# Performance work log

Hardware: AMD Instinct MI355X
Metric: run time of the kernel (lower is better)

## Reference

```python
import jax, jax.numpy as jnp
import numpy as np

N, FIN, H, C, D = 50000, 128, 4, 64, 4
E = 800000


def leaky_relu(x, slope):
    return jnp.where(x >= 0, x, slope * x)


def gat_layer(x, src, dst, W, A, att_src, att_dst, bias):
    # x: [N, Fin]; W: [Fin, H*C]; A: [Fin, H*D]; att_*: [H, D]; bias: [C]
    n = x.shape[0]
    h = (x @ W).reshape(n, H, -1)          # [N, H, C] message features
    a = (x @ A).reshape(n, H, -1)          # [N, H, D] attention features
    alpha_src = jnp.einsum('nhd,hd->nh', a, att_src)   # [N, H]
    alpha_dst = jnp.einsum('nhd,hd->nh', a, att_dst)   # [N, H]
    e = leaky_relu(alpha_src[src] + alpha_dst[dst], 0.2)  # [E, H]
    # edge softmax over incoming edges of each destination node
    m = jax.ops.segment_max(e, dst, num_segments=n)       # [N, H]
    ex = jnp.exp(e - m[dst])                               # [E, H]
    denom = jax.ops.segment_sum(ex, dst, num_segments=n)  # [N, H]
    w = ex / denom[dst]                                    # [E, H]
    msg = h[src] * w[..., None]                            # [E, H, C]
    out = jax.ops.segment_sum(msg, dst, num_segments=n)   # [N, H, C]
    return out.mean(axis=1) + bias                         # head-average -> [N, C]


def setup_inputs() -> dict:
    key = jax.random.key(0)
    ks = jax.random.split(key, 12)
    x = jax.random.normal(ks[0], (N, FIN), dtype=jnp.float32)
    edge_index = jax.random.randint(ks[1], (2, E), 0, N, dtype=jnp.int64)
    s = 0.05
    return {
        'x': x,
        'edge_index': edge_index,
        'W1': jax.random.normal(ks[2], (FIN, H * C), dtype=jnp.float32) * s,
        'A1': jax.random.normal(ks[3], (FIN, H * D), dtype=jnp.float32) * s,
        'att_src1': jax.random.normal(ks[4], (H, D), dtype=jnp.float32) * s,
        'att_dst1': jax.random.normal(ks[5], (H, D), dtype=jnp.float32) * s,
        'b1': jnp.zeros((C,), dtype=jnp.float32),
        'W2': jax.random.normal(ks[6], (C, H * C), dtype=jnp.float32) * s,
        'A2': jax.random.normal(ks[7], (C, H * D), dtype=jnp.float32) * s,
        'att_src2': jax.random.normal(ks[8], (H, D), dtype=jnp.float32) * s,
        'att_dst2': jax.random.normal(ks[9], (H, D), dtype=jnp.float32) * s,
        'b2': jnp.zeros((C,), dtype=jnp.float32),
    }


def reference(x, edge_index, W1, A1, att_src1, att_dst1, b1, W2, A2, att_src2, att_dst2, b2):
    src, dst = edge_index[0], edge_index[1]
    x = gat_layer(x, src, dst, W1, A1, att_src1, att_dst1, b1)
    x = leaky_relu(x, 0.1)
    x = gat_layer(x, src, dst, W2, A2, att_src2, att_dst2, b2)
    x = leaky_relu(x, 0.1)
    return x
```

## Files before the change

kernel.cpp:

```cpp
#include <hip/hip_runtime.h>


#define N_NODES 50000
#define N_EDGES 800000
#define CAP 64
#define NB_SC4 782
#define NB_NODE1 782

typedef __attribute__((ext_vector_type(8))) short short8;
typedef __attribute__((ext_vector_type(8))) _Float16 f16x8;
typedef __attribute__((ext_vector_type(4))) float f32x4;
typedef __attribute__((ext_vector_type(8))) unsigned short ushort8;
typedef __attribute__((ext_vector_type(4))) unsigned short us4v;

__device__ __forceinline__ float bf2f(unsigned short u){
  return __uint_as_float(((unsigned int)u) << 16);
}
__device__ __forceinline__ unsigned short f2bf(float f){
  unsigned int u = __float_as_uint(f);
  u = (u + 0x7FFFu + ((u >> 16) & 1u)) >> 16;
  return (unsigned short)u;
}
__device__ __forceinline__ float ldf(const void* p, int i, bool bf){
  return bf ? bf2f(((const unsigned short*)p)[i]) : ((const float*)p)[i];
}

struct SetupPtrs {
  const void *W1, *A1, *aS1, *aD1, *b1, *W2, *A2, *aS2, *aD2, *b2, *x;
};

__global__ __launch_bounds__(256) void k_setup(SetupPtrs S,
    _Float16* __restrict__ Wb1f, _Float16* __restrict__ Wb2f,
    unsigned short* __restrict__ Bsd1f, unsigned short* __restrict__ Bsd2f,
    float* __restrict__ bc1, float* __restrict__ bc2,
    int* __restrict__ flag)
{
  __shared__ int sbf;
  const int tid = threadIdx.x;
  if (tid < 64){
    unsigned int w = ((const unsigned int*)S.x)[tid] & 0xFFFFu;
    unsigned int e = (w >> 7) & 0xFFu;
    bool hit = (e >= 100u && e <= 135u);
    unsigned long long m = __ballot(hit);
    if (tid == 0) sbf = (__popcll(m) > 40) ? 1 : 0;
  }
  __syncthreads();
  const bool bf = (sbf != 0);
  const int bw = blockIdx.x;
  if (bw < 128){
    int t = bw * 256 + tid;
    int j = t & 7, lane = (t >> 3) & 63, kt = (t >> 9) & 15, nt = t >> 13;
    int q = kt * 32 + (lane >> 4) * 8 + j;
    int c = nt * 16 + (lane & 15);
    int h = q >> 7, f = q & 127;
    Wb1f[t] = (_Float16)(0.25f * ldf(S.W1, f * 256 + h * 64 + c, bf));
  } else if (bw < 192){
    int t = (bw - 128) * 256 + tid;
    int j = t & 7, lane = (t >> 3) & 63, kt = (t >> 9) & 7, nt = t >> 12;
    int q = kt * 32 + (lane >> 4) * 8 + j;
    int c = nt * 16 + (lane & 15);
    int h = q >> 6, f = q & 63;
    Wb2f[t] = (_Float16)(0.25f * ldf(S.W2, f * 256 + h * 64 + c, bf));
  } else if (bw < 200){
    int t = (bw - 192) * 256 + tid;
    int j = t & 7, lane = (t >> 3) & 63, kt = t >> 9;
    int k = kt * 32 + (lane >> 4) * 8 + j;
    int c = lane & 15;
    float v = 0.f;
    if (c < 4){
      for (int dd = 0; dd < 4; ++dd)
        v += ldf(S.A1, k * 16 + c * 4 + dd, bf) * ldf(S.aS1, c * 4 + dd, bf);
    } else if (c < 8){
      int h = c - 4;
      for (int dd = 0; dd < 4; ++dd)
        v += ldf(S.A1, k * 16 + h * 4 + dd, bf) * ldf(S.aD1, h * 4 + dd, bf);
    }
    Bsd1f[t] = f2bf(v);
  } else if (bw < 204){
    int t = (bw - 200) * 256 + tid;
    int j = t & 7, lane = (t >> 3) & 63, kt = t >> 9;
    int k = kt * 32 + (lane >> 4) * 8 + j;
    int c = lane & 15;
    float v = 0.f;
    if (c < 4){
      for (int dd = 0; dd < 4; ++dd)
        v += ldf(S.A2, k * 16 + c * 4 + dd, bf) * ldf(S.aS2, c * 4 + dd, bf);
    } else if (c < 8){
      int h = c - 4;
      for (int dd = 0; dd < 4; ++dd)
        v += ldf(S.A2, k * 16 + h * 4 + dd, bf) * ldf(S.aD2, h * 4 + dd, bf);
    }
    Bsd2f[t] = f2bf(v);
  } else {
    if (tid < 64)       bc1[tid] = ldf(S.b1, tid, bf);
    else if (tid < 128) bc2[tid - 64] = ldf(S.b2, tid - 64, bf);
    else if (tid == 128) *flag = bf ? 1 : 0;
  }
}


template<int F, bool DYN>
__device__ __forceinline__ void nodeA_body(int nblk, int tid,
    const void* __restrict__ xin_, const unsigned short* __restrict__ Bsdf,
    float* __restrict__ alpha_s, float* __restrict__ alpha_d,
    const int* __restrict__ flag)
{
  const int STR = F + 8;
  const int KT  = F / 32;
  const int CH  = F / 8;
  __shared__ unsigned short xs[64 * (F + 8)];
  const int base = nblk * 64;
  bool bf = true;
  if (DYN) bf = (*flag != 0);
  for (int v = tid; v < 64 * CH; v += 256){
    int row = v / CH, c8 = v % CH;
    int node = base + row; if (node >= N_NODES) node = N_NODES - 1;
    size_t g = (size_t)node * F + c8 * 8;
    ushort8 u;
    if (!DYN || bf){
      u = *(const ushort8*)((const unsigned short*)xin_ + g);
    } else {
      const float* xf = (const float*)xin_ + g;
      float4 f0 = *(const float4*)xf, f1 = *(const float4*)(xf + 4);
      u[0]=f2bf(f0.x); u[1]=f2bf(f0.y); u[2]=f2bf(f0.z); u[3]=f2bf(f0.w);
      u[4]=f2bf(f1.x); u[5]=f2bf(f1.y); u[6]=f2bf(f1.z); u[7]=f2bf(f1.w);
    }
    *(ushort8*)&xs[row * STR + c8 * 8] = u;
  }
  __syncthreads();

  const int wave = tid >> 6, l = tid & 63;
  const int quad = l >> 4, m = l & 15;
  const int wbase = base + wave * 16;

  f32x4 aacc = (f32x4)0.f;
  #pragma unroll
  for (int kt = 0; kt < KT; ++kt){
    short8 af = *(const short8*)&xs[(wave * 16 + m) * STR + kt * 32 + quad * 8];
    short8 sdfrag = *(const short8*)(Bsdf + ((size_t)kt * 64 + l) * 8);
    aacc = __builtin_amdgcn_mfma_f32_16x16x32_bf16(af, sdfrag, aacc, 0, 0, 0);
  }
  if (m < 8){
    float* dstp = (m < 4) ? alpha_s : alpha_d;
    int hh = m & 3;
    #pragma unroll
    for (int r = 0; r < 4; ++r){
      int node = wbase + quad * 4 + r;
      if (node < N_NODES) dstp[node * 4 + hh] = aacc[r];
    }
  }
}


__global__ __launch_bounds__(256) void k_scatter_nodeA1(
    const int* __restrict__ src, const int* __restrict__ dst,
    int* __restrict__ fill, unsigned short* __restrict__ csr,
    const void* __restrict__ xin_, const unsigned short* __restrict__ Bsdf,
    float* __restrict__ alpha_s, float* __restrict__ alpha_d,
    const int* __restrict__ flag)
{
  const int b = blockIdx.x, tid = threadIdx.x;
  if (b < NB_SC4){
    const int ebase = b * 1024 + tid;
    int d[4], s[4];
    #pragma unroll
    for (int i = 0; i < 4; ++i){
      int e = ebase + i * 256;
      bool ok = (e < N_EDGES);
      d[i] = ok ? dst[e] : -1;
      s[i] = ok ? src[e] : 0;
    }
    #pragma unroll
    for (int i = 0; i < 4; ++i){
      if (d[i] >= 0){
        int r = atomicAdd(&fill[d[i]], 1);
        if (r < CAP) csr[((unsigned)d[i] << 6) + r] = (unsigned short)s[i];
      }
    }
    return;
  }
  nodeA_body<128, true>(b - NB_SC4, tid, xin_, Bsdf, alpha_s, alpha_d, flag);
}

template<int F, bool DYN>
__global__ __launch_bounds__(256) void k_nodeA(const void* __restrict__ xin_,
    const unsigned short* __restrict__ Bsdf,
    float* __restrict__ alpha_s, float* __restrict__ alpha_d,
    const int* __restrict__ flag)
{
  nodeA_body<F, DYN>(blockIdx.x, threadIdx.x, xin_, Bsdf, alpha_s, alpha_d, flag);
}


template<int FIN, bool BF>
__device__ __forceinline__ void ldrow(const void* xg, unsigned s, int f0,
                                      float (&out)[FIN / 16])
{
  const int NFL = FIN / 16;
  if (BF){
    const unsigned short* p = (const unsigned short*)xg + (size_t)s * FIN + f0;
    if (NFL == 8){
      ushort8 u = *(const ushort8*)p;
      #pragma unroll
      for (int j = 0; j < NFL; ++j) out[j] = bf2f(u[j]);
    } else {
      us4v u = *(const us4v*)p;
      #pragma unroll
      for (int j = 0; j < NFL; ++j) out[j] = bf2f(u[j]);
    }
  } else {
    const float* p = (const float*)xg + (size_t)s * FIN + f0;
    #pragma unroll
    for (int j = 0; j < NFL; ++j) out[j] = p[j];
  }
}

template<int FIN, bool BF, int STR>
__device__ __forceinline__ void aggr_phase1(const void* __restrict__ xg,
    const float* __restrict__ alpha_s, const float* __restrict__ alpha_d,
    const int* __restrict__ fill, const unsigned short* __restrict__ csr,
    _Float16* __restrict__ ylds, int base, int w, int l)
{
  const int NFL = FIN / 16;
  const int h = l >> 4, sub = l & 15, f0 = sub * NFL;
  #pragma unroll 1
  for (int r = 0; r < 4; ++r){
    const int n = base + w * 4 + r;
    const float adv = alpha_d[n * 4 + h];
    float den = 0.f;
    float acc[NFL];
    #pragma unroll
    for (int j = 0; j < NFL; ++j) acc[j] = 0.f;

    int cnt = fill[n]; if (cnt > CAP) cnt = CAP;
    const unsigned short* cp = csr + ((unsigned)n << 6);
    int p = 0;
    for (; p + 8 <= cnt; p += 8){
      ushort8 s8 = *(const ushort8*)(cp + p);
      float a[8];
      float v[8][NFL];
      #pragma unroll
      for (int i = 0; i < 8; ++i){
        unsigned s = s8[i];
        a[i] = alpha_s[s * 4 + h];
        ldrow<FIN, BF>(xg, s, f0, v[i]);
      }
      #pragma unroll
      for (int i = 0; i < 8; ++i){
        float e = a[i] + adv; e = fmaxf(e, 0.2f * e); float wt = __expf(e);
        den += wt;
        #pragma unroll
        for (int j = 0; j < NFL; ++j) acc[j] += wt * v[i][j];
      }
    }
    if (p + 4 <= cnt){
      ushort4 s4 = *(const ushort4*)(cp + p);
      unsigned sx = s4.x, sy = s4.y, sz = s4.z, sw = s4.w;
      float ax = alpha_s[sx * 4 + h];
      float ay = alpha_s[sy * 4 + h];
      float az = alpha_s[sz * 4 + h];
      float aw = alpha_s[sw * 4 + h];
      float vx[NFL], vy[NFL], vz[NFL], vw[NFL];
      ldrow<FIN, BF>(xg, sx, f0, vx);
      ldrow<FIN, BF>(xg, sy, f0, vy);
      ldrow<FIN, BF>(xg, sz, f0, vz);
      ldrow<FIN, BF>(xg, sw, f0, vw);
      float e0 = ax + adv; e0 = fmaxf(e0, 0.2f * e0); float w0 = __expf(e0);
      float e1 = ay + adv; e1 = fmaxf(e1, 0.2f * e1); float w1 = __expf(e1);
      float e2 = az + adv; e2 = fmaxf(e2, 0.2f * e2); float w2 = __expf(e2);
      float e3 = aw + adv; e3 = fmaxf(e3, 0.2f * e3); float w3 = __expf(e3);
      den += w0; den += w1; den += w2; den += w3;
      #pragma unroll
      for (int j = 0; j < NFL; ++j)
        acc[j] += w0 * vx[j] + w1 * vy[j] + w2 * vz[j] + w3 * vw[j];
      p += 4;
    }
    for (; p < cnt; ++p){
      unsigned s = cp[p];
      float a = alpha_s[s * 4 + h];
      float v0[NFL];
      ldrow<FIN, BF>(xg, s, f0, v0);
      float e = a + adv; e = fmaxf(e, 0.2f * e); float wgt = __expf(e);
      den += wgt;
      #pragma unroll
      for (int j = 0; j < NFL; ++j) acc[j] += wgt * v0[j];
    }
    const float rh = (den > 0.f) ? (1.f / den) : 0.f;
    const int row = w * 4 + r;
    _Float16* yp = &ylds[row * STR + h * FIN + f0];
    #pragma unroll
    for (int j = 0; j < NFL; ++j) yp[j] = (_Float16)(acc[j] * rh);
  }
}

template<int FIN, int MODE>
__global__ __launch_bounds__(256) void k_aggrX(
    const void* __restrict__ xg,
    const float* __restrict__ alpha_s, const float* __restrict__ alpha_d,
    const int* __restrict__ fill, const unsigned short* __restrict__ csr,
    const _Float16* __restrict__ Wf,
    const float* __restrict__ bias, void* __restrict__ out,
    const int* __restrict__ flag)
{
  const int K = 4 * FIN, KT = K / 32, STR = K + 8;
  __shared__ _Float16 ylds[16 * (4 * FIN + 8)];
  const int tid = threadIdx.x, w = tid >> 6, l = tid & 63;
  const int base = blockIdx.x * 16;

  if (MODE == 0 && *flag == 0)
    aggr_phase1<FIN, false, STR>(xg, alpha_s, alpha_d, fill, csr, ylds, base, w, l);
  else
    aggr_phase1<FIN, true,  STR>(xg, alpha_s, alpha_d, fill, csr, ylds, base, w, l);
  __syncthreads();

  const int quad = l >> 4, m = l & 15;
  const int nt = w;
  f32x4 cacc = (f32x4)0.f;
  #pragma unroll
  for (int kt = 0; kt < KT; ++kt){
    f16x8 av = *(const f16x8*)&ylds[m * STR + kt * 32 + quad * 8];
    f16x8 bv = *(const f16x8*)(Wf + ((size_t)(nt * KT + kt) * 64 + l) * 8);
    cacc = __builtin_amdgcn_mfma_f32_16x16x32_f16(av, bv, cacc, 0, 0, 0);
  }
  const int c = nt * 16 + m;
  const float bs = bias[c];
  #pragma unroll
  for (int r2 = 0; r2 < 4; ++r2){
    int node = base + quad * 4 + r2;
    float v = cacc[r2] + bs;
    v = fmaxf(v, 0.1f * v);
    if (MODE == 0){
      ((unsigned short*)out)[(size_t)node * 64 + c] = f2bf(v);
    } else {
      if (*flag) ((unsigned short*)out)[(size_t)node * 64 + c] = f2bf(v);
      else       ((float*)out)[(size_t)node * 64 + c] = v;
    }
  }
}


extern "C" void kernel_launch(void* const* d_in, const int* in_sizes, int n_in,
                              void* d_out, int out_size, void* d_ws, size_t ws_size,
                              hipStream_t stream)
{
  const void* x  = d_in[0];
  const int* ei  = (const int*)d_in[1];
  const int* src = ei;
  const int* dst = ei + N_EDGES;

  char* ws = (char*)d_ws;
  unsigned short* csr = (unsigned short*)(ws);
  unsigned short* x2  = (unsigned short*)(ws + 6400000);
  float* as_    = (float*)(ws + 12800000);
  float* ad_    = (float*)(ws + 13600000);
  int*   fill   = (int*)  (ws + 14400000);
  _Float16* Wb1f = (_Float16*)(ws + 14600000);
  _Float16* Wb2f = (_Float16*)(ws + 14665536);
  unsigned short* Bsd1f = (unsigned short*)(ws + 14698304);
  unsigned short* Bsd2f = (unsigned short*)(ws + 14702400);
  float* bc1    = (float*)(ws + 14704448);
  float* bc2    = (float*)(ws + 14704704);
  int*   flag   = (int*)  (ws + 14704960);

  hipMemsetAsync(fill, 0, N_NODES * sizeof(int), stream);

  SetupPtrs S;
  S.W1 = d_in[2];  S.A1 = d_in[3];  S.aS1 = d_in[4];  S.aD1 = d_in[5];  S.b1 = d_in[6];
  S.W2 = d_in[7];  S.A2 = d_in[8];  S.aS2 = d_in[9];  S.aD2 = d_in[10]; S.b2 = d_in[11];
  S.x  = x;
  k_setup<<<205, 256, 0, stream>>>(S, Wb1f, Wb2f, Bsd1f, Bsd2f, bc1, bc2, flag);

  k_scatter_nodeA1<<<NB_SC4 + NB_NODE1, 256, 0, stream>>>(
      src, dst, fill, csr, x, Bsd1f, as_, ad_, flag);

  k_aggrX<128, 0><<<N_NODES / 16, 256, 0, stream>>>(
      x, as_, ad_, fill, csr, Wb1f, bc1, x2, flag);

  k_nodeA<64, false><<<NB_NODE1, 256, 0, stream>>>(x2, Bsd2f, as_, ad_, flag);

  k_aggrX<64, 1><<<N_NODES / 16, 256, 0, stream>>>(
      x2, as_, ad_, fill, csr, Wb2f, bc2, d_out, flag);
}
```

Before: 291.5 us.

## Merge setup into scatter kernel and fuse layer-2 attention logits into aggregation epilogue

The separate setup kernel is folded into the scatter/nodeA1 kernel. Each nodeA1 block now recomputes the layer-1 attention projection matrix into LDS and detects the input dtype itself, so it no longer depends on the setup output. The standalone layer-2 nodeA kernel is removed: the layer-1 aggregation epilogue stages its bf16 output tile in LDS and one wave computes alpha_src/alpha_dst for layer 2, written to new buffers. This drops two launches and a re-read of x2, at the cost of redundant per-block projection work and an extra barrier and serial tail in the aggregation kernel.

Result: slower. 298.9 us (+2.5%).

```diff
diff --git a/kernel.cpp b/kernel.cpp
--- a/kernel.cpp
+++ b/kernel.cpp
@@ -6,6 +6,7 @@
 #define CAP 64
 #define NB_SC4 782
 #define NB_NODE1 782
+#define NB_SETUP 197
 
 typedef __attribute__((ext_vector_type(8))) short short8;
 typedef __attribute__((ext_vector_type(8))) _Float16 f16x8;
@@ -29,14 +30,123 @@
   const void *W1, *A1, *aS1, *aD1, *b1, *W2, *A2, *aS2, *aD2, *b2, *x;
 };
 
-__global__ __launch_bounds__(256) void k_setup(SetupPtrs S,
+
+__device__ __forceinline__ void nodeA1_body(int nblk, int tid,
+    const void* __restrict__ xin_, const void* __restrict__ A1,
+    const void* __restrict__ aS1, const void* __restrict__ aD1,
+    float* __restrict__ alpha_s, float* __restrict__ alpha_d)
+{
+  const int F = 128, STR = F + 8, KT = 4, CH = F / 8;
+  __shared__ unsigned short xs[64 * 136];
+  __shared__ unsigned short BsdL[2048];
+  __shared__ int sbf;
+  const int base = nblk * 64;
+  if (tid < 64){
+    unsigned int wv = ((const unsigned int*)xin_)[tid] & 0xFFFFu;
+    unsigned int ex = (wv >> 7) & 0xFFu;
+    bool hit = (ex >= 100u && ex <= 135u);
+    unsigned long long mm = __ballot(hit);
+    if (tid == 0) sbf = (__popcll(mm) > 40) ? 1 : 0;
+  }
+  __syncthreads();
+  const bool bf = (sbf != 0);
+
+  {
+    const int lane = tid & 63, kt = tid >> 6, c = lane & 15;
+    ushort8 v8;
+    #pragma unroll
+    for (int j = 0; j < 8; ++j){
+      int k = kt * 32 + (lane >> 4) * 8 + j;
+      float v = 0.f;
+      if (c < 4){
+        #pragma unroll
+        for (int dd = 0; dd < 4; ++dd)
+          v += ldf(A1, k * 16 + c * 4 + dd, bf) * ldf(aS1, c * 4 + dd, bf);
+      } else if (c < 8){
+        int hh = c - 4;
+        #pragma unroll
+        for (int dd = 0; dd < 4; ++dd)
+          v += ldf(A1, k * 16 + hh * 4 + dd, bf) * ldf(aD1, hh * 4 + dd, bf);
+      }
+      v8[j] = f2bf(v);
+    }
+    *(ushort8*)&BsdL[tid * 8] = v8;
+  }
+
+  for (int v = tid; v < 64 * CH; v += 256){
+    int row = v / CH, c8 = v % CH;
+    int node = base + row; if (node >= N_NODES) node = N_NODES - 1;
+    size_t g = (size_t)node * F + c8 * 8;
+    ushort8 u;
+    if (bf){
+      u = *(const ushort8*)((const unsigned short*)xin_ + g);
+    } else {
+      const float* xf = (const float*)xin_ + g;
+      float4 f0 = *(const float4*)xf, f1 = *(const float4*)(xf + 4);
+      u[0]=f2bf(f0.x); u[1]=f2bf(f0.y); u[2]=f2bf(f0.z); u[3]=f2bf(f0.w);
+      u[4]=f2bf(f1.x); u[5]=f2bf(f1.y); u[6]=f2bf(f1.z); u[7]=f2bf(f1.w);
+    }
+    *(ushort8*)&xs[row * STR + c8 * 8] = u;
+  }
+  __syncthreads();
+
+  const int wave = tid >> 6, l = tid & 63;
+  const int quad = l >> 4, m = l & 15;
+  const int wbase = base + wave * 16;
+
+  f32x4 aacc = (f32x4)0.f;
+  #pragma unroll
+  for (int kt = 0; kt < KT; ++kt){
+    short8 af = *(const short8*)&xs[(wave * 16 + m) * STR + kt * 32 + quad * 8];
+    short8 sd = *(const short8*)&BsdL[((size_t)kt * 64 + l) * 8];
+    aacc = __builtin_amdgcn_mfma_f32_16x16x32_bf16(af, sd, aacc, 0, 0, 0);
+  }
+  if (m < 8){
+    float* dstp = (m < 4) ? alpha_s : alpha_d;
+    int hh = m & 3;
+    #pragma unroll
+    for (int r = 0; r < 4; ++r){
+      int node = wbase + quad * 4 + r;
+      if (node < N_NODES) dstp[node * 4 + hh] = aacc[r];
+    }
+  }
+}
+
+
+__global__ __launch_bounds__(256) void k_mega(SetupPtrs S,
+    const int* __restrict__ src, const int* __restrict__ dst,
+    int* __restrict__ fill, unsigned short* __restrict__ csr,
+    float* __restrict__ alpha_s, float* __restrict__ alpha_d,
     _Float16* __restrict__ Wb1f, _Float16* __restrict__ Wb2f,
-    unsigned short* __restrict__ Bsd1f, unsigned short* __restrict__ Bsd2f,
+    unsigned short* __restrict__ Bsd2f,
     float* __restrict__ bc1, float* __restrict__ bc2,
     int* __restrict__ flag)
 {
+  const int b = blockIdx.x, tid = threadIdx.x;
+  if (b < NB_SC4){
+    const int ebase = b * 1024 + tid;
+    int d[4], s[4];
+    #pragma unroll
+    for (int i = 0; i < 4; ++i){
+      int e = ebase + i * 256;
+      bool ok = (e < N_EDGES);
+      d[i] = ok ? dst[e] : -1;
+      s[i] = ok ? src[e] : 0;
+    }
+    #pragma unroll
+    for (int i = 0; i < 4; ++i){
+      if (d[i] >= 0){
+        int r = atomicAdd(&fill[d[i]], 1);
+        if (r < CAP) csr[((unsigned)d[i] << 6) + r] = (unsigned short)s[i];
+      }
+    }
+    return;
+  }
+  if (b < NB_SC4 + NB_NODE1){
+    nodeA1_body(b - NB_SC4, tid, S.x, S.A1, S.aS1, S.aD1, alpha_s, alpha_d);
+    return;
+  }
   __shared__ int sbf;
-  const int tid = threadIdx.x;
   if (tid < 64){
     unsigned int w = ((const unsigned int*)S.x)[tid] & 0xFFFFu;
     unsigned int e = (w >> 7) & 0xFFu;
@@ -46,7 +156,7 @@
   }
   __syncthreads();
   const bool bf = (sbf != 0);
-  const int bw = blockIdx.x;
+  const int bw = b - NB_SC4 - NB_NODE1;
   if (bw < 128){
     int t = bw * 256 + tid;
     int j = t & 7, lane = (t >> 3) & 63, kt = (t >> 9) & 15, nt = t >> 13;
@@ -61,23 +171,8 @@
     int c = nt * 16 + (lane & 15);
     int h = q >> 6, f = q & 63;
     Wb2f[t] = (_Float16)(0.25f * ldf(S.W2, f * 256 + h * 64 + c, bf));
-  } else if (bw < 200){
+  } else if (bw < 196){
     int t = (bw - 192) * 256 + tid;
-    int j = t & 7, lane = (t >> 3) & 63, kt = t >> 9;
-    int k = kt * 32 + (lane >> 4) * 8 + j;
-    int c = lane & 15;
-    float v = 0.f;
-    if (c < 4){
-      for (int dd = 0; dd < 4; ++dd)
-        v += ldf(S.A1, k * 16 + c * 4 + dd, bf) * ldf(S.aS1, c * 4 + dd, bf);
-    } else if (c < 8){
-      int h = c - 4;
-      for (int dd = 0; dd < 4; ++dd)
-        v += ldf(S.A1, k * 16 + h * 4 + dd, bf) * ldf(S.aD1, h * 4 + dd, bf);
-    }
-    Bsd1f[t] = f2bf(v);
-  } else if (bw < 204){
-    int t = (bw - 200) * 256 + tid;
     int j = t & 7, lane = (t >> 3) & 63, kt = t >> 9;
     int k = kt * 32 + (lane >> 4) * 8 + j;
     int c = lane & 15;
@@ -96,99 +191,6 @@
     else if (tid < 128) bc2[tid - 64] = ldf(S.b2, tid - 64, bf);
     else if (tid == 128) *flag = bf ? 1 : 0;
   }
-}
-
-
-template<int F, bool DYN>
-__device__ __forceinline__ void nodeA_body(int nblk, int tid,
-    const void* __restrict__ xin_, const unsigned short* __restrict__ Bsdf,
-    float* __restrict__ alpha_s, float* __restrict__ alpha_d,
-    const int* __restrict__ flag)
-{
-  const int STR = F + 8;
-  const int KT  = F / 32;
-  const int CH  = F / 8;
-  __shared__ unsigned short xs[64 * (F + 8)];
-  const int base = nblk * 64;
-  bool bf = true;
-  if (DYN) bf = (*flag != 0);
-  for (int v = tid; v < 64 * CH; v += 256){
-    int row = v / CH, c8 = v % CH;
-    int node = base + row; if (node >= N_NODES) node = N_NODES - 1;
-    size_t g = (size_t)node * F + c8 * 8;
-    ushort8 u;
-    if (!DYN || bf){
-      u = *(const ushort8*)((const unsigned short*)xin_ + g);
-    } else {
-      const float* xf = (const float*)xin_ + g;
-      float4 f0 = *(const float4*)xf, f1 = *(const float4*)(xf + 4);
-      u[0]=f2bf(f0.x); u[1]=f2bf(f0.y); u[2]=f2bf(f0.z); u[3]=f2bf(f0.w);
-      u[4]=f2bf(f1.x); u[5]=f2bf(f1.y); u[6]=f2bf(f1.z); u[7]=f2bf(f1.w);
-    }
-    *(ushort8*)&xs[row * STR + c8 * 8] = u;
-  }
-  __syncthreads();
-
-  const int wave = tid >> 6, l = tid & 63;
-  const int quad = l >> 4, m = l & 15;
-  const int wbase = base + wave * 16;
-
-  f32x4 aacc = (f32x4)0.f;
-  #pragma unroll
-  for (int kt = 0; kt < KT; ++kt){
-    short8 af = *(const short8*)&xs[(wave * 16 + m) * STR + kt * 32 + quad * 8];
-    short8 sdfrag = *(const short8*)(Bsdf + ((size_t)kt * 64 + l) * 8);
-    aacc = __builtin_amdgcn_mfma_f32_16x16x32_bf16(af, sdfrag, aacc, 0, 0, 0);
-  }
-  if (m < 8){
-    float* dstp = (m < 4) ? alpha_s : alpha_d;
-    int hh = m & 3;
-    #pragma unroll
-    for (int r = 0; r < 4; ++r){
-      int node = wbase + quad * 4 + r;
-      if (node < N_NODES) dstp[node * 4 + hh] = aacc[r];
-    }
-  }
-}
-
-
-__global__ __launch_bounds__(256) void k_scatter_nodeA1(
-    const int* __restrict__ src, const int* __restrict__ dst,
-    int* __restrict__ fill, unsigned short* __restrict__ csr,
-    const void* __restrict__ xin_, const unsigned short* __restrict__ Bsdf,
-    float* __restrict__ alpha_s, float* __restrict__ alpha_d,
-    const int* __restrict__ flag)
-{
-  const int b = blockIdx.x, tid = threadIdx.x;
-  if (b < NB_SC4){
-    const int ebase = b * 1024 + tid;
-    int d[4], s[4];
-    #pragma unroll
-    for (int i = 0; i < 4; ++i){
-      int e = ebase + i * 256;
-      bool ok = (e < N_EDGES);
-      d[i] = ok ? dst[e] : -1;
-      s[i] = ok ? src[e] : 0;
-    }
-    #pragma unroll
-    for (int i = 0; i < 4; ++i){
-      if (d[i] >= 0){
-        int r = atomicAdd(&fill[d[i]], 1);
-        if (r < CAP) csr[((unsigned)d[i] << 6) + r] = (unsigned short)s[i];
-      }
-    }
-    return;
-  }
-  nodeA_body<128, true>(b - NB_SC4, tid, xin_, Bsdf, alpha_s, alpha_d, flag);
-}
-
-template<int F, bool DYN>
-__global__ __launch_bounds__(256) void k_nodeA(const void* __restrict__ xin_,
-    const unsigned short* __restrict__ Bsdf,
-    float* __restrict__ alpha_s, float* __restrict__ alpha_d,
-    const int* __restrict__ flag)
-{
-  nodeA_body<F, DYN>(blockIdx.x, threadIdx.x, xin_, Bsdf, alpha_s, alpha_d, flag);
 }
 
 
@@ -300,10 +302,13 @@
     const int* __restrict__ fill, const unsigned short* __restrict__ csr,
     const _Float16* __restrict__ Wf,
     const float* __restrict__ bias, void* __restrict__ out,
-    const int* __restrict__ flag)
+    const int* __restrict__ flag,
+    const unsigned short* __restrict__ Bsd2f,
+    float* __restrict__ as2, float* __restrict__ ad2)
 {
   const int K = 4 * FIN, KT = K / 32, STR = K + 8;
   __shared__ _Float16 ylds[16 * (4 * FIN + 8)];
+  __shared__ unsigned short x2t[16 * 72];
   const int tid = threadIdx.x, w = tid >> 6, l = tid & 63;
   const int base = blockIdx.x * 16;
 
@@ -330,10 +335,34 @@
     float v = cacc[r2] + bs;
     v = fmaxf(v, 0.1f * v);
     if (MODE == 0){
-      ((unsigned short*)out)[(size_t)node * 64 + c] = f2bf(v);
+      unsigned short o = f2bf(v);
+      ((unsigned short*)out)[(size_t)node * 64 + c] = o;
+      x2t[(quad * 4 + r2) * 72 + c] = o;
     } else {
       if (*flag) ((unsigned short*)out)[(size_t)node * 64 + c] = f2bf(v);
       else       ((float*)out)[(size_t)node * 64 + c] = v;
+    }
+  }
+
+  if (MODE == 0){
+    __syncthreads();
+    if (w == 0){
+      f32x4 aacc = (f32x4)0.f;
+      #pragma unroll
+      for (int kt = 0; kt < 2; ++kt){
+        short8 af = *(const short8*)&x2t[m * 72 + kt * 32 + quad * 8];
+        short8 sd = *(const short8*)(Bsd2f + ((size_t)kt * 64 + l) * 8);
+        aacc = __builtin_amdgcn_mfma_f32_16x16x32_bf16(af, sd, aacc, 0, 0, 0);
+      }
+      if (m < 8){
+        float* dstp = (m < 4) ? as2 : ad2;
+        int hh = m & 3;
+        #pragma unroll
+        for (int r = 0; r < 4; ++r){
+          int node = base + quad * 4 + r;
+          dstp[node * 4 + hh] = aacc[r];
+        }
+      }
     }
   }
 }
@@ -353,14 +382,15 @@
   unsigned short* x2  = (unsigned short*)(ws + 6400000);
   float* as_    = (float*)(ws + 12800000);
   float* ad_    = (float*)(ws + 13600000);
-  int*   fill   = (int*)  (ws + 14400000);
-  _Float16* Wb1f = (_Float16*)(ws + 14600000);
-  _Float16* Wb2f = (_Float16*)(ws + 14665536);
-  unsigned short* Bsd1f = (unsigned short*)(ws + 14698304);
-  unsigned short* Bsd2f = (unsigned short*)(ws + 14702400);
-  float* bc1    = (float*)(ws + 14704448);
-  float* bc2    = (float*)(ws + 14704704);
-  int*   flag   = (int*)  (ws + 14704960);
+  float* as2_   = (float*)(ws + 14400000);
+  float* ad2_   = (float*)(ws + 15200000);
+  int*   fill   = (int*)  (ws + 16000000);
+  _Float16* Wb1f = (_Float16*)(ws + 16200000);
+  _Float16* Wb2f = (_Float16*)(ws + 16265536);
+  unsigned short* Bsd2f = (unsigned short*)(ws + 16298304);
+  float* bc1    = (float*)(ws + 16300352);
+  float* bc2    = (float*)(ws + 16300608);
+  int*   flag   = (int*)  (ws + 16300864);
 
   hipMemsetAsync(fill, 0, N_NODES * sizeof(int), stream);
 
@@ -368,16 +398,13 @@
   S.W1 = d_in[2];  S.A1 = d_in[3];  S.aS1 = d_in[4];  S.aD1 = d_in[5];  S.b1 = d_in[6];
   S.W2 = d_in[7];  S.A2 = d_in[8];  S.aS2 = d_in[9];  S.aD2 = d_in[10]; S.b2 = d_in[11];
   S.x  = x;
-  k_setup<<<205, 256, 0, stream>>>(S, Wb1f, Wb2f, Bsd1f, Bsd2f, bc1, bc2, flag);
-
-  k_scatter_nodeA1<<<NB_SC4 + NB_NODE1, 256, 0, stream>>>(
-      src, dst, fill, csr, x, Bsd1f, as_, ad_, flag);
+
+  k_mega<<<NB_SC4 + NB_NODE1 + NB_SETUP, 256, 0, stream>>>(
+      S, src, dst, fill, csr, as_, ad_, Wb1f, Wb2f, Bsd2f, bc1, bc2, flag);
 
   k_aggrX<128, 0><<<N_NODES / 16, 256, 0, stream>>>(
-      x, as_, ad_, fill, csr, Wb1f, bc1, x2, flag);
-
-  k_nodeA<64, false><<<NB_NODE1, 256, 0, stream>>>(x2, Bsd2f, as_, ad_, flag);
+      x, as_, ad_, fill, csr, Wb1f, bc1, x2, flag, Bsd2f, as2_, ad2_);
 
   k_aggrX<64, 1><<<N_NODES / 16, 256, 0, stream>>>(
-      x2, as_, ad_, fill, csr, Wb2f, bc2, d_out, flag);
-}
+      x2, as2_, ad2_, fill, csr, Wb2f, bc2, d_out, flag, Bsd2f, as2_, ad2_);
+}
```
